# Kernel tuning notes

Hardware: AMD Instinct MI355X
Metric: run time of the kernel (lower is better)

Reference implementation:

```python
import jax, jax.numpy as jnp
import numpy as np

N_NODES = 50000
N_EDGES = 650000
NEG_SLOPE = 0.2


def gat_conv(x, src, dst, W, a_src, a_dst, bias, concat):
    """PyG-style GATConv (eval mode, self-loops already included in src/dst).
    x: [N, F_in], W: [F_in, H*C], a_src/a_dst: [H, C], bias: [H*C] or [C]."""
    N = x.shape[0]
    H, C = a_src.shape
    h = (x @ W).reshape(N, H, C)                      # [N, H, C]
    al_src = (h * a_src).sum(-1)                      # [N, H]
    al_dst = (h * a_dst).sum(-1)                      # [N, H]
    logits = jax.nn.leaky_relu(al_src[src] + al_dst[dst], NEG_SLOPE)  # [E, H]
    # segment softmax over destination neighborhoods
    m = jax.ops.segment_max(logits, dst, num_segments=N)
    m = jnp.where(jnp.isfinite(m), m, 0.0)
    e = jnp.exp(logits - m[dst])
    s = jax.ops.segment_sum(e, dst, num_segments=N)
    alpha = e / (s[dst] + 1e-16)                      # [E, H]
    msg = alpha[:, :, None] * h[src]                  # [E, H, C]
    out = jax.ops.segment_sum(msg, dst, num_segments=N)  # [N, H, C]
    out = out.reshape(N, H * C) if concat else out.mean(axis=1)
    return out + bias


def setup_inputs() -> dict:
    key = jax.random.key(0)
    ks = jax.random.split(key, 16)
    IN, HID, H, OUT = 128, 64, 4, 1
    x = jax.random.normal(ks[0], (N_NODES, IN), dtype=jnp.float32)
    edge_index = jax.random.randint(ks[1], (2, N_EDGES), 0, N_NODES, dtype=jnp.int64)
    s = 0.1
    params = {
        'W1': jax.random.normal(ks[2], (IN, H * HID), dtype=jnp.float32) * s,
        'a_src1': jax.random.normal(ks[3], (H, HID), dtype=jnp.float32) * s,
        'a_dst1': jax.random.normal(ks[4], (H, HID), dtype=jnp.float32) * s,
        'b1': jnp.zeros((H * HID,), dtype=jnp.float32),
        'W2': jax.random.normal(ks[5], (H * HID, H * HID), dtype=jnp.float32) * s,
        'a_src2': jax.random.normal(ks[6], (H, HID), dtype=jnp.float32) * s,
        'a_dst2': jax.random.normal(ks[7], (H, HID), dtype=jnp.float32) * s,
        'b2': jnp.zeros((H * HID,), dtype=jnp.float32),
        'W3': jax.random.normal(ks[8], (H * HID, OUT), dtype=jnp.float32) * s,
        'a_src3': jax.random.normal(ks[9], (1, OUT), dtype=jnp.float32) * s,
        'a_dst3': jax.random.normal(ks[10], (1, OUT), dtype=jnp.float32) * s,
        'b3': jnp.zeros((OUT,), dtype=jnp.float32),
    }
    return {'x': x, 'edge_index': edge_index, **params}


def reference(x, edge_index, W1, a_src1, a_dst1, b1, W2, a_src2, a_dst2, b2, W3, a_src3, a_dst3, b3):
    N = x.shape[0]
    loops = jnp.arange(N, dtype=edge_index.dtype)
    src = jnp.concatenate([edge_index[0], loops])
    dst = jnp.concatenate([edge_index[1], loops])
    h = gat_conv(x, src, dst, W1, a_src1, a_dst1, b1, concat=True)
    h = jax.nn.elu(h)  # dropout: identity in eval mode
    h = gat_conv(h, src, dst, W2, a_src2, a_dst2, b2, concat=True)
    h = jax.nn.elu(h)
    out = gat_conv(h, src, dst, W3, a_src3, a_dst3, b3, concat=False)
    return out
```

## Files before the change

### kernel.cpp

```cpp
#include <hip/hip_runtime.h>
#include <math.h>

#define NN 50000
#define NE 650000
#define NET 700000
#define FD 256
#define NEG 0.2f
#define NB 49

static __device__ __forceinline__ float lrelu(float v){ return v > 0.f ? v : NEG*v; }

static __device__ __forceinline__ unsigned short f2bf(float f){
  union { float f; unsigned u; } v; v.f = f;
  unsigned r = v.u + 0x7fff + ((v.u >> 16) & 1);
  return (unsigned short)(r >> 16);
}
static __device__ __forceinline__ float bf2f(unsigned short h){
  union { unsigned u; float f; } v; v.u = ((unsigned)h) << 16;
  return v.f;
}
static __device__ __forceinline__ float bflo(unsigned u){ return __uint_as_float(u << 16); }
static __device__ __forceinline__ float bfhi(unsigned u){ return __uint_as_float(u & 0xffff0000u); }

static __device__ __forceinline__ void gload_lds16(const unsigned short* g, unsigned short* l){
  __builtin_amdgcn_global_load_lds(
      (const __attribute__((address_space(1))) unsigned int*)(g),
      (__attribute__((address_space(3))) unsigned int*)(l), 16, 0, 0);
}

typedef __attribute__((ext_vector_type(8))) short short8_t;
typedef __attribute__((ext_vector_type(4))) float f32x4;

#define NX (NN*128)
#define CAST_ELEMS (NX + 128*256 + 256*256)
#define CAST_BLOCKS ((CAST_ELEMS/4 + 255)/256)
#define CNT_BLOCKS ((NET + 255)/256)
__global__ void init_fused(const float* __restrict__ x, const float* __restrict__ W1,
                           const float* __restrict__ W2,
                           unsigned short* __restrict__ xh, unsigned short* __restrict__ xl,
                           unsigned short* __restrict__ bt1h, unsigned short* __restrict__ bt1l,
                           unsigned short* __restrict__ bt2h, unsigned short* __restrict__ bt2l,
                           const int* __restrict__ ei, int* __restrict__ deg){
  int b = blockIdx.x;
  if (b >= CAST_BLOCKS){
    int e = (b - CAST_BLOCKS)*256 + threadIdx.x;
    if (e < NET){
      int d = (e < NE) ? ei[NE + e] : (e - NE);
      atomicAdd(&deg[d], 1);
    }
    return;
  }
  int i = (b*256 + threadIdx.x)*4;
  if (i < NX){
    float4 f = *(const float4*)(x + i);
    ushort4 h, l;
    h.x = f2bf(f.x); l.x = f2bf(f.x - bf2f(h.x));
    h.y = f2bf(f.y); l.y = f2bf(f.y - bf2f(h.y));
    h.z = f2bf(f.z); l.z = f2bf(f.z - bf2f(h.z));
    h.w = f2bf(f.w); l.w = f2bf(f.w - bf2f(h.w));
    *(ushort4*)(xh + i) = h;
    *(ushort4*)(xl + i) = l;
    return;
  }
  int e, K;
  const float* B;
  unsigned short *bh, *bl;
  if (i < NX + 128*256){ e = i - NX; K = 128; B = W1; bh = bt1h; bl = bt1l; }
  else if (i < CAST_ELEMS){ e = i - NX - 128*256; K = 256; B = W2; bh = bt2h; bl = bt2l; }
  else return;
  int k = e >> 8, n = e & 255;
  float4 f = *(const float4*)(B + e);
  #pragma unroll
  for (int j=0;j<4;j++){
    float fv = (j==0)?f.x:(j==1)?f.y:(j==2)?f.z:f.w;
    unsigned short h = f2bf(fv);
    bh[(n+j)*K + k] = h;
    bl[(n+j)*K + k] = f2bf(fv - bf2f(h));
  }
}

__global__ void scan_block(const int* __restrict__ deg, int* __restrict__ excl, int* __restrict__ bsums){
  __shared__ int sh[256];
  int t = threadIdx.x;
  int i0 = blockIdx.x*1024 + t*4;
  int v0 = (i0+0 < NN) ? deg[i0+0] : 0;
  int v1 = (i0+1 < NN) ? deg[i0+1] : 0;
  int v2 = (i0+2 < NN) ? deg[i0+2] : 0;
  int v3 = (i0+3 < NN) ? deg[i0+3] : 0;
  int tot = v0+v1+v2+v3;
  sh[t] = tot;
  __syncthreads();
  for (int off=1; off<256; off<<=1){
    int x = (t>=off) ? sh[t-off] : 0;
    __syncthreads();
    sh[t] += x;
    __syncthreads();
  }
  int base = sh[t] - tot;
  if (i0+0 < NN) excl[i0+0] = base;
  if (i0+1 < NN) excl[i0+1] = base + v0;
  if (i0+2 < NN) excl[i0+2] = base + v0+v1;
  if (i0+3 < NN) excl[i0+3] = base + v0+v1+v2;
  if (t == 255) bsums[blockIdx.x] = sh[255];
}

__global__ void scan_add(int* __restrict__ indptr, const int* __restrict__ bsums, int* __restrict__ cursor){
  __shared__ int boff[64];
  if (threadIdx.x < 64){
    int lane = threadIdx.x;
    int v = (lane < NB) ? bsums[lane] : 0;
    int orig = v;
    for (int off=1; off<64; off<<=1){
      int u = __shfl_up(v, off);
      if (lane >= off) v += u;
    }
    boff[lane] = v - orig;
  }
  __syncthreads();
  int i = blockIdx.x*blockDim.x + threadIdx.x;
  if (i < NN){
    int v = indptr[i] + boff[i>>10];
    indptr[i] = v;
    cursor[i] = v;
  }
  if (i == 0) indptr[NN] = NET;
}

__global__ void scatter_csr(const int* __restrict__ ei, int* __restrict__ cursor, int* __restrict__ csr){
  int e = blockIdx.x*blockDim.x + threadIdx.x;
  if (e >= NET) return;
  int s, d;
  if (e < NE){ s = ei[e]; d = ei[NE+e]; } else { s = e-NE; d = e-NE; }
  int pos = atomicAdd(&cursor[d], 1);
  csr[pos] = s;
}

template<int K>
__global__ __launch_bounds__(256, 3) void gemm_mfma(const unsigned short* __restrict__ Ahg,
                                                    const unsigned short* __restrict__ Alg,
                                                    const unsigned short* __restrict__ Bth,
                                                    const unsigned short* __restrict__ Btl,
                                                    unsigned short* __restrict__ Cb,
                                                    const float* __restrict__ a_src,
                                                    const float* __restrict__ a_dst,
                                                    float* __restrict__ al,
                                                    int M){
  constexpr int ITERS = K/32;
  __shared__ unsigned short Ah[128*32], Al[128*32], Bh[128*32], Bl[128*32];
  int t = threadIdx.x;
  int wave = t >> 6, lane = t & 63;
  int wm = wave >> 1, wn = wave & 1;
  int quad = lane >> 4, l16 = lane & 15;
  int bm0 = blockIdx.y*128, bn0 = blockIdx.x*128;

  const unsigned short* gsrc = (wave==0)?Ahg:(wave==1)?Alg:(wave==2)?Bth:Btl;
  unsigned short* lbuf       = (wave==0)?Ah :(wave==1)?Al :(wave==2)?Bh :Bl;
  int sbase = (wave < 2) ? bm0 : bn0;
  int srow = lane >> 2;
  int skg  = (lane & 3) * 8;

  const unsigned short* gp[8];
  #pragma unroll
  for (int i=0;i<8;i++){
    int r = sbase + i*16 + srow;
    if (wave < 2) r = min(r, M-1);
    gp[i] = gsrc + (size_t)r*K + skg;
  }

  f32x4 acc[4][4];
  #pragma unroll
  for (int i=0;i<4;i++)
    #pragma unroll
    for (int j=0;j<4;j++) acc[i][j] = (f32x4){0.f,0.f,0.f,0.f};

  #pragma unroll
  for (int i=0;i<8;i++) gload_lds16(gp[i], lbuf + i*512);

  #pragma unroll
  for (int it=0; it<ITERS; ++it){
    __syncthreads();

    short8_t afh[4], afl[4], bfh[4], bfl[4];
    #pragma unroll
    for (int mt=0; mt<4; ++mt){
      int row = wm*64 + mt*16 + l16;
      afh[mt] = *(short8_t*)&Ah[row*32 + quad*8];
      afl[mt] = *(short8_t*)&Al[row*32 + quad*8];
    }
    #pragma unroll
    for (int nt=0; nt<4; ++nt){
      int col = wn*64 + nt*16 + l16;
      bfh[nt] = *(short8_t*)&Bh[col*32 + quad*8];
      bfl[nt] = *(short8_t*)&Bl[col*32 + quad*8];
    }
    __syncthreads();

    if (it+1 < ITERS){
      int k0 = (it+1)*32;
      #pragma unroll
      for (int i=0;i<8;i++) gload_lds16(gp[i] + k0, lbuf + i*512);
    }

    #pragma unroll
    for (int mt=0; mt<4; ++mt)
      #pragma unroll
      for (int nt=0; nt<4; ++nt){
        acc[mt][nt] = __builtin_amdgcn_mfma_f32_16x16x32_bf16(afh[mt], bfh[nt], acc[mt][nt], 0,0,0);
        acc[mt][nt] = __builtin_amdgcn_mfma_f32_16x16x32_bf16(afh[mt], bfl[nt], acc[mt][nt], 0,0,0);
        acc[mt][nt] = __builtin_amdgcn_mfma_f32_16x16x32_bf16(afl[mt], bfh[nt], acc[mt][nt], 0,0,0);
      }
  }

  int head_w = (bn0 >> 6) + wn;
  float cs[4], cd[4];
  #pragma unroll
  for (int nt=0; nt<4; ++nt){
    cs[nt] = a_src[head_w*64 + nt*16 + l16];
    cd[nt] = a_dst[head_w*64 + nt*16 + l16];
  }
  {
    float* fsc = (float*)lbuf;
    int grow = bm0 + wm*64 + lane;
    #pragma unroll
    for (int pass=0; pass<2; ++pass){
      #pragma unroll
      for (int mt=0; mt<4; ++mt)
        #pragma unroll
        for (int r=0; r<4; ++r){
          float p = 0.f;
          #pragma unroll
          for (int nt=0; nt<4; ++nt)
            p += acc[mt][nt][r] * (pass ? cd[nt] : cs[nt]);
          fsc[(mt*16 + quad*4 + r)*17 + l16] = p;
        }
      float s = 0.f;
      #pragma unroll
      for (int j=0; j<16; ++j) s += fsc[lane*17 + j];
      if (grow < M) al[grow*8 + pass*4 + head_w] = s;
    }
  }

  unsigned short* tile = lbuf;
  #pragma unroll
  for (int mt=0; mt<4; ++mt)
    #pragma unroll
    for (int r=0; r<4; ++r){
      int rl = mt*16 + quad*4 + r;
      #pragma unroll
      for (int nt=0; nt<4; ++nt)
        tile[rl*64 + nt*16 + l16] = f2bf(acc[mt][nt][r]);
    }
  int orow = lane >> 3, ocol = (lane & 7) * 8;
  #pragma unroll
  for (int it=0; it<8; ++it){
    int rl = it*8 + orow;
    int row = bm0 + wm*64 + rl;
    if (row < M){
      uint4 v = *(uint4*)&tile[rl*64 + ocol];
      *(uint4*)(Cb + (size_t)row*FD + bn0 + wn*64 + ocol) = v;
    }
  }
}

template<bool FUSE_W3>
__global__ __launch_bounds__(256) void gat_agg(const unsigned short* __restrict__ hb,
                                               const float* __restrict__ al,
                                               const int* __restrict__ indptr, const int* __restrict__ csr,
                                               const float* __restrict__ bias,
                                               unsigned short* __restrict__ outh,
                                               unsigned short* __restrict__ outl,
                                               const float* __restrict__ W3,
                                               float* __restrict__ h3){
  __shared__ float ebuf[8][128];
  __shared__ int   sbuf[8][32];
  int wave = threadIdx.x >> 6, lane = threadIdx.x & 63;
  int half = lane >> 5, l32 = lane & 31;
  int slot = wave*2 + half;
  int n = blockIdx.x*8 + slot;
  if (n >= NN) return;
  int head8 = l32 >> 3;
  int2 ip = *(const int2*)(indptr + n);
  int base = ip.x, deg = ip.y - ip.x;
  float4 ald = *(const float4*)(al + n*8 + 4);
  float* eb = &ebuf[slot][0];
  int*   sb = &sbuf[slot][0];
  const char* hp = (const char*)hb + l32*16;

  float acc[8] = {0.f,0.f,0.f,0.f,0.f,0.f,0.f,0.f};
  float4 esum = make_float4(0.f,0.f,0.f,0.f);

  for (int j0 = 0; j0 < deg; j0 += 32){
    int j = j0 + l32;
    float4 e4 = make_float4(0.f,0.f,0.f,0.f);
    int sj = 0;
    if (j < deg){
      sj = csr[base + j];
      float4 als = *(const float4*)(al + sj*8);
      e4.x = __expf(lrelu(als.x + ald.x));
      e4.y = __expf(lrelu(als.y + ald.y));
      e4.z = __expf(lrelu(als.z + ald.z));
      e4.w = __expf(lrelu(als.w + ald.w));
      esum.x += e4.x; esum.y += e4.y; esum.z += e4.z; esum.w += e4.w;
    }
    *(float4*)&eb[l32*4] = e4;
    sb[l32] = sj << 9;
    int cnt  = min(32, deg - j0);
    int cpad = (cnt + 7) & ~7;
    for (int tt = 0; tt < cpad; tt += 8){
      uint4 r[8];
      float v[8];
      #pragma unroll
      for (int q=0; q<8; ++q){
        int o = sb[tt+q];
        v[q] = eb[(tt+q)*4 + head8];
        r[q] = *(const uint4*)(hp + o);
      }
      #pragma unroll
      for (int q=0; q<8; ++q){
        acc[0]+=v[q]*bflo(r[q].x); acc[1]+=v[q]*bfhi(r[q].x);
        acc[2]+=v[q]*bflo(r[q].y); acc[3]+=v[q]*bfhi(r[q].y);
        acc[4]+=v[q]*bflo(r[q].z); acc[5]+=v[q]*bfhi(r[q].z);
        acc[6]+=v[q]*bflo(r[q].w); acc[7]+=v[q]*bfhi(r[q].w);
      }
    }
  }

  for (int off=16; off; off>>=1){
    esum.x += __shfl_xor(esum.x, off);
    esum.y += __shfl_xor(esum.y, off);
    esum.z += __shfl_xor(esum.z, off);
    esum.w += __shfl_xor(esum.w, off);
  }
  float sH = (head8==0)?esum.x:(head8==1)?esum.y:(head8==2)?esum.z:esum.w;
  float inv = 1.f/(sH + 1e-16f);
  int ch0 = l32*8;
  float4 b0 = *(const float4*)(bias + ch0);
  float4 b1 = *(const float4*)(bias + ch0 + 4);
  float o[8];
  o[0]=acc[0]*inv+b0.x; o[1]=acc[1]*inv+b0.y; o[2]=acc[2]*inv+b0.z; o[3]=acc[3]*inv+b0.w;
  o[4]=acc[4]*inv+b1.x; o[5]=acc[5]*inv+b1.y; o[6]=acc[6]*inv+b1.z; o[7]=acc[7]*inv+b1.w;
  #pragma unroll
  for (int i=0;i<8;i++) o[i] = o[i] > 0.f ? o[i] : expm1f(o[i]);

  if (FUSE_W3){
    float4 w0 = *(const float4*)(W3 + ch0);
    float4 w1 = *(const float4*)(W3 + ch0 + 4);
    float p = o[0]*w0.x + o[1]*w0.y + o[2]*w0.z + o[3]*w0.w
            + o[4]*w1.x + o[5]*w1.y + o[6]*w1.z + o[7]*w1.w;
    #pragma unroll
    for (int off=16; off; off>>=1) p += __shfl_xor(p, off);
    if (l32 == 0) h3[n] = p;
  } else {
    unsigned hi[4], lo[4];
    #pragma unroll
    for (int i=0;i<4;i++){
      unsigned short h0 = f2bf(o[2*i]),   h1 = f2bf(o[2*i+1]);
      unsigned short g0 = f2bf(o[2*i]   - bf2f(h0));
      unsigned short g1 = f2bf(o[2*i+1] - bf2f(h1));
      hi[i] = (unsigned)h0 | ((unsigned)h1 << 16);
      lo[i] = (unsigned)g0 | ((unsigned)g1 << 16);
    }
    *(uint4*)(outh + (size_t)n*FD + ch0) = make_uint4(hi[0],hi[1],hi[2],hi[3]);
    *(uint4*)(outl + (size_t)n*FD + ch0) = make_uint4(lo[0],lo[1],lo[2],lo[3]);
  }
}

__global__ __launch_bounds__(256) void gat_agg3(const float* __restrict__ h3, const int* __restrict__ indptr,
                                                const int* __restrict__ csr, const float* __restrict__ asrc,
                                                const float* __restrict__ adst, const float* __restrict__ b3,
                                                float* __restrict__ out){
  int tid = blockIdx.x*blockDim.x + threadIdx.x;
  int n = tid >> 2, sub = tid & 3;
  if (n >= NN) return;
  float as = asrc[0], ad = adst[0];
  float hd = h3[n]*ad;
  int2 ip = *(const int2*)(indptr + n);
  float s = 0.f, w = 0.f;
  for (int e = ip.x + sub; e < ip.y; e += 4){
    float hv = h3[csr[e]];
    float ee = __expf(lrelu(as*hv + hd));
    s += ee; w += ee*hv;
  }
  s += __shfl_xor(s, 1); w += __shfl_xor(w, 1);
  s += __shfl_xor(s, 2); w += __shfl_xor(w, 2);
  if (sub == 0) out[n] = w/(s + 1e-16f) + b3[0];
}

extern "C" void kernel_launch(void* const* d_in, const int* in_sizes, int n_in,
                              void* d_out, int out_size, void* d_ws, size_t ws_size,
                              hipStream_t stream){
  const float* x   = (const float*)d_in[0];
  const int*   ei  = (const int*)d_in[1];
  const float* W1  = (const float*)d_in[2];
  const float* as1 = (const float*)d_in[3];
  const float* ad1 = (const float*)d_in[4];
  const float* b1  = (const float*)d_in[5];
  const float* W2  = (const float*)d_in[6];
  const float* as2 = (const float*)d_in[7];
  const float* ad2 = (const float*)d_in[8];
  const float* b2  = (const float*)d_in[9];
  const float* W3  = (const float*)d_in[10];
  const float* as3 = (const float*)d_in[11];
  const float* ad3 = (const float*)d_in[12];
  const float* b3  = (const float*)d_in[13];
  float* outp = (float*)d_out;

  char* w = (char*)d_ws;
  size_t off = 0;
  auto alloc = [&](size_t bytes)->void*{
    void* p = w + off; off += (bytes + 255) & ~(size_t)255; return p;
  };
  unsigned short* hb  = (unsigned short*)alloc((size_t)NN*FD*2);
  unsigned short* oh  = (unsigned short*)alloc((size_t)NN*FD*2);
  unsigned short* ol  = (unsigned short*)alloc((size_t)NN*FD*2);
  unsigned short* xh  = (unsigned short*)alloc((size_t)NN*128*2);
  unsigned short* xl  = (unsigned short*)alloc((size_t)NN*128*2);
  float* al    = (float*)alloc((size_t)NN*8*4);
  int*   indptr= (int*)alloc((size_t)(NN+1)*4);
  int*   cursor= (int*)alloc((size_t)NN*4);
  int*   csr   = (int*)alloc((size_t)NET*4);
  int*   bsums = (int*)alloc(64*4);
  float* h3    = (float*)alloc((size_t)NN*4);
  unsigned short* bt1h = (unsigned short*)alloc((size_t)256*128*2);
  unsigned short* bt1l = (unsigned short*)alloc((size_t)256*128*2);
  unsigned short* bt2h = (unsigned short*)alloc((size_t)256*256*2);
  unsigned short* bt2l = (unsigned short*)alloc((size_t)256*256*2);

  hipMemsetAsync(cursor, 0, (size_t)NN*4, stream);
  init_fused<<<CAST_BLOCKS + CNT_BLOCKS, 256, 0, stream>>>(x, W1, W2, xh, xl,
                                                           bt1h, bt1l, bt2h, bt2l,
                                                           ei, cursor);
  scan_block<<<NB, 256, 0, stream>>>(cursor, indptr, bsums);
  scan_add<<<(NN+255)/256, 256, 0, stream>>>(indptr, bsums, cursor);
  scatter_csr<<<(NET+255)/256, 256, 0, stream>>>(ei, cursor, csr);

  dim3 gemm_grid(FD/128, (NN+127)/128);
  int agg_blocks = (NN+7)/8;

  gemm_mfma<128><<<gemm_grid, 256, 0, stream>>>(xh, xl, bt1h, bt1l, hb, as1, ad1, al, NN);
  gat_agg<false><<<agg_blocks, 256, 0, stream>>>(hb, al, indptr, csr, b1, oh, ol, nullptr, nullptr);
  gemm_mfma<256><<<gemm_grid, 256, 0, stream>>>(oh, ol, bt2h, bt2l, hb, as2, ad2, al, NN);
  gat_agg<true><<<agg_blocks, 256, 0, stream>>>(hb, al, indptr, csr, b2, nullptr, nullptr, W3, h3);
  gat_agg3<<<(NN*4+255)/256, 256, 0, stream>>>(h3, indptr, csr, as3, ad3, b3, outp);
}
```

Measured before the change: 341.0 us.

## Store features in 32-channel groups and split aggregation across channel groups

The GEMM now writes node features in a channel-group-major layout (8 groups of 32 channels, each [N,32]) and attention logits head-major. Aggregation runs one block per (node tile, channel group), so each half-wave gathers a contiguous 64-byte row slice per neighbor for a single head. The intent is better cache locality, because each group's feature table is smaller. In exchange every edge's index and attention value is reloaded and recomputed 8 times, the output stores become scalar, and the fused W3 projection needs atomics plus a memset of h3.

```diff
diff --git a/kernel.cpp b/kernel.cpp
--- a/kernel.cpp
+++ b/kernel.cpp
@@ -236,7 +236,7 @@
       float s = 0.f;
       #pragma unroll
       for (int j=0; j<16; ++j) s += fsc[lane*17 + j];
-      if (grow < M) al[grow*8 + pass*4 + head_w] = s;
+      if (grow < M) al[(size_t)(pass*4 + head_w)*NN + grow] = s;
     }
   }
 
@@ -251,13 +251,15 @@
         tile[rl*64 + nt*16 + l16] = f2bf(acc[mt][nt][r]);
     }
   int orow = lane >> 3, ocol = (lane & 7) * 8;
+  int ch = bn0 + wn*64 + ocol;
+  int g = ch >> 5;
   #pragma unroll
   for (int it=0; it<8; ++it){
     int rl = it*8 + orow;
     int row = bm0 + wm*64 + rl;
     if (row < M){
       uint4 v = *(uint4*)&tile[rl*64 + ocol];
-      *(uint4*)(Cb + (size_t)row*FD + bn0 + wn*64 + ocol) = v;
+      *(uint4*)(Cb + ((size_t)g*NN + row)*32 + (ch & 31)) = v;
     }
   }
 }
@@ -271,97 +273,66 @@
                                                unsigned short* __restrict__ outl,
                                                const float* __restrict__ W3,
                                                float* __restrict__ h3){
-  __shared__ float ebuf[8][128];
+  __shared__ float ebuf[8][32];
   __shared__ int   sbuf[8][32];
   int wave = threadIdx.x >> 6, lane = threadIdx.x & 63;
   int half = lane >> 5, l32 = lane & 31;
   int slot = wave*2 + half;
-  int n = blockIdx.x*8 + slot;
+  int g    = blockIdx.x & 7;
+  int tile = blockIdx.x >> 3;
+  int n = tile*8 + slot;
   if (n >= NN) return;
-  int head8 = l32 >> 3;
+  int head = g >> 1;
   int2 ip = *(const int2*)(indptr + n);
   int base = ip.x, deg = ip.y - ip.x;
-  float4 ald = *(const float4*)(al + n*8 + 4);
+  float ald = al[(size_t)(4 + head)*NN + n];
+  const float* als_p = al + (size_t)head*NN;
   float* eb = &ebuf[slot][0];
   int*   sb = &sbuf[slot][0];
-  const char* hp = (const char*)hb + l32*16;
-
-  float acc[8] = {0.f,0.f,0.f,0.f,0.f,0.f,0.f,0.f};
-  float4 esum = make_float4(0.f,0.f,0.f,0.f);
-
+  const unsigned short* hg = hb + (size_t)g*NN*32 + l32;
+
+  float acc = 0.f, esum = 0.f;
   for (int j0 = 0; j0 < deg; j0 += 32){
     int j = j0 + l32;
-    float4 e4 = make_float4(0.f,0.f,0.f,0.f);
-    int sj = 0;
+    float e = 0.f; int sj = 0;
     if (j < deg){
-      sj = csr[base + j];
-      float4 als = *(const float4*)(al + sj*8);
-      e4.x = __expf(lrelu(als.x + ald.x));
-      e4.y = __expf(lrelu(als.y + ald.y));
-      e4.z = __expf(lrelu(als.z + ald.z));
-      e4.w = __expf(lrelu(als.w + ald.w));
-      esum.x += e4.x; esum.y += e4.y; esum.z += e4.z; esum.w += e4.w;
-    }
-    *(float4*)&eb[l32*4] = e4;
-    sb[l32] = sj << 9;
+      sj = __builtin_nontemporal_load(csr + base + j);
+      float as = als_p[sj];
+      e = __expf(lrelu(as + ald));
+      esum += e;
+    }
+    eb[l32] = e;
+    sb[l32] = sj << 5;
     int cnt  = min(32, deg - j0);
     int cpad = (cnt + 7) & ~7;
     for (int tt = 0; tt < cpad; tt += 8){
-      uint4 r[8];
-      float v[8];
-      #pragma unroll
-      for (int q=0; q<8; ++q){
-        int o = sb[tt+q];
-        v[q] = eb[(tt+q)*4 + head8];
-        r[q] = *(const uint4*)(hp + o);
-      }
-      #pragma unroll
-      for (int q=0; q<8; ++q){
-        acc[0]+=v[q]*bflo(r[q].x); acc[1]+=v[q]*bfhi(r[q].x);
-        acc[2]+=v[q]*bflo(r[q].y); acc[3]+=v[q]*bfhi(r[q].y);
-        acc[4]+=v[q]*bflo(r[q].z); acc[5]+=v[q]*bfhi(r[q].z);
-        acc[6]+=v[q]*bflo(r[q].w); acc[7]+=v[q]*bfhi(r[q].w);
-      }
-    }
-  }
-
-  for (int off=16; off; off>>=1){
-    esum.x += __shfl_xor(esum.x, off);
-    esum.y += __shfl_xor(esum.y, off);
-    esum.z += __shfl_xor(esum.z, off);
-    esum.w += __shfl_xor(esum.w, off);
-  }
-  float sH = (head8==0)?esum.x:(head8==1)?esum.y:(head8==2)?esum.z:esum.w;
-  float inv = 1.f/(sH + 1e-16f);
-  int ch0 = l32*8;
-  float4 b0 = *(const float4*)(bias + ch0);
-  float4 b1 = *(const float4*)(bias + ch0 + 4);
-  float o[8];
-  o[0]=acc[0]*inv+b0.x; o[1]=acc[1]*inv+b0.y; o[2]=acc[2]*inv+b0.z; o[3]=acc[3]*inv+b0.w;
-  o[4]=acc[4]*inv+b1.x; o[5]=acc[5]*inv+b1.y; o[6]=acc[6]*inv+b1.z; o[7]=acc[7]*inv+b1.w;
-  #pragma unroll
-  for (int i=0;i<8;i++) o[i] = o[i] > 0.f ? o[i] : expm1f(o[i]);
+      int   ofs[8]; float vv[8];
+      #pragma unroll
+      for (int q=0; q<8; ++q){ ofs[q] = sb[tt+q]; vv[q] = eb[tt+q]; }
+      float hv[8];
+      #pragma unroll
+      for (int q=0; q<8; ++q) hv[q] = bf2f(hg[ofs[q]]);
+      #pragma unroll
+      for (int q=0; q<8; ++q) acc += vv[q]*hv[q];
+    }
+  }
+
+  for (int off=16; off; off>>=1) esum += __shfl_xor(esum, off);
+  float inv = 1.f/(esum + 1e-16f);
+  int ch = g*32 + l32;
+  float o = acc*inv + bias[ch];
+  o = o > 0.f ? o : expm1f(o);
 
   if (FUSE_W3){
-    float4 w0 = *(const float4*)(W3 + ch0);
-    float4 w1 = *(const float4*)(W3 + ch0 + 4);
-    float p = o[0]*w0.x + o[1]*w0.y + o[2]*w0.z + o[3]*w0.w
-            + o[4]*w1.x + o[5]*w1.y + o[6]*w1.z + o[7]*w1.w;
+    float p = o * W3[ch];
     #pragma unroll
     for (int off=16; off; off>>=1) p += __shfl_xor(p, off);
-    if (l32 == 0) h3[n] = p;
+    if (l32 == 0) atomicAdd(&h3[n], p);
   } else {
-    unsigned hi[4], lo[4];
-    #pragma unroll
-    for (int i=0;i<4;i++){
-      unsigned short h0 = f2bf(o[2*i]),   h1 = f2bf(o[2*i+1]);
-      unsigned short g0 = f2bf(o[2*i]   - bf2f(h0));
-      unsigned short g1 = f2bf(o[2*i+1] - bf2f(h1));
-      hi[i] = (unsigned)h0 | ((unsigned)h1 << 16);
-      lo[i] = (unsigned)g0 | ((unsigned)g1 << 16);
-    }
-    *(uint4*)(outh + (size_t)n*FD + ch0) = make_uint4(hi[0],hi[1],hi[2],hi[3]);
-    *(uint4*)(outl + (size_t)n*FD + ch0) = make_uint4(lo[0],lo[1],lo[2],lo[3]);
+    unsigned short hh = f2bf(o);
+    unsigned short ll = f2bf(o - bf2f(hh));
+    __builtin_nontemporal_store(hh, outh + (size_t)n*FD + ch);
+    __builtin_nontemporal_store(ll, outl + (size_t)n*FD + ch);
   }
 }
 
@@ -427,6 +398,7 @@
   unsigned short* bt2l = (unsigned short*)alloc((size_t)256*256*2);
 
   hipMemsetAsync(cursor, 0, (size_t)NN*4, stream);
+  hipMemsetAsync(h3, 0, (size_t)NN*4, stream);
   init_fused<<<CAST_BLOCKS + CNT_BLOCKS, 256, 0, stream>>>(x, W1, W2, xh, xl,
                                                            bt1h, bt1l, bt2h, bt2l,
                                                            ei, cursor);
@@ -435,7 +407,7 @@
   scatter_csr<<<(NET+255)/256, 256, 0, stream>>>(ei, cursor, csr);
 
   dim3 gemm_grid(FD/128, (NN+127)/128);
-  int agg_blocks = (NN+7)/8;
+  int agg_blocks = (NN/8) * 8;
 
   gemm_mfma<128><<<gemm_grid, 256, 0, stream>>>(xh, xl, bt1h, bt1l, hb, as1, ad1, al, NN);
   gat_agg<false><<<agg_blocks, 256, 0, stream>>>(hb, al, indptr, csr, b1, oh, ol, nullptr, nullptr);
```

Result: slower. 446.8 us (+31.0%).

## Precompute per-edge attention exponentials in a separate edge-parallel kernel

Applied to the files above, without the earlier changes.

Adds an alpha_k kernel that computes exp(leaky_relu(al_src+al_dst)) for every CSR edge in an edge-parallel pass, storing the results in a float4 buffer. To support this, scatter_csr now also records each edge's destination. gat_agg then reads the precomputed values instead of gathering al[src] and computing exponentials inside its node-parallel loop. This splits the gather latency away from the aggregation kernel, at the cost of two extra launches, an extra edge-sized write and read, and a second CSR array.

```diff
diff --git a/kernel.cpp b/kernel.cpp
--- a/kernel.cpp
+++ b/kernel.cpp
@@ -4,6 +4,7 @@
 #define NN 50000
 #define NE 650000
 #define NET 700000
+#define NETP (NET + 16)
 #define FD 256
 #define NEG 0.2f
 #define NB 49
@@ -126,13 +127,30 @@
   if (i == 0) indptr[NN] = NET;
 }
 
-__global__ void scatter_csr(const int* __restrict__ ei, int* __restrict__ cursor, int* __restrict__ csr){
+__global__ void scatter_csr(const int* __restrict__ ei, int* __restrict__ cursor,
+                            int* __restrict__ csr, int* __restrict__ csrd){
   int e = blockIdx.x*blockDim.x + threadIdx.x;
   if (e >= NET) return;
   int s, d;
   if (e < NE){ s = ei[e]; d = ei[NE+e]; } else { s = e-NE; d = e-NE; }
   int pos = atomicAdd(&cursor[d], 1);
   csr[pos] = s;
+  csrd[pos] = d;
+}
+
+__global__ __launch_bounds__(256) void alpha_k(const int* __restrict__ csr, const int* __restrict__ csrd,
+                                               const float* __restrict__ al, float4* __restrict__ alpha4){
+  int p = blockIdx.x*256 + threadIdx.x;
+  if (p >= NET) return;
+  int s = csr[p], d = csrd[p];
+  float4 as = *(const float4*)(al + s*8);
+  float4 ad = *(const float4*)(al + d*8 + 4);
+  float4 e;
+  e.x = __expf(lrelu(as.x + ad.x));
+  e.y = __expf(lrelu(as.y + ad.y));
+  e.z = __expf(lrelu(as.z + ad.z));
+  e.w = __expf(lrelu(as.w + ad.w));
+  alpha4[p] = e;
 }
 
 template<int K>
@@ -264,7 +282,7 @@
 
 template<bool FUSE_W3>
 __global__ __launch_bounds__(256) void gat_agg(const unsigned short* __restrict__ hb,
-                                               const float* __restrict__ al,
+                                               const float4* __restrict__ alpha4,
                                                const int* __restrict__ indptr, const int* __restrict__ csr,
                                                const float* __restrict__ bias,
                                                unsigned short* __restrict__ outh,
@@ -281,7 +299,6 @@
   int head8 = l32 >> 3;
   int2 ip = *(const int2*)(indptr + n);
   int base = ip.x, deg = ip.y - ip.x;
-  float4 ald = *(const float4*)(al + n*8 + 4);
   float* eb = &ebuf[slot][0];
   int*   sb = &sbuf[slot][0];
   const char* hp = (const char*)hb + l32*16;
@@ -295,11 +312,7 @@
     int sj = 0;
     if (j < deg){
       sj = csr[base + j];
-      float4 als = *(const float4*)(al + sj*8);
-      e4.x = __expf(lrelu(als.x + ald.x));
-      e4.y = __expf(lrelu(als.y + ald.y));
-      e4.z = __expf(lrelu(als.z + ald.z));
-      e4.w = __expf(lrelu(als.w + ald.w));
+      e4 = alpha4[base + j];
       esum.x += e4.x; esum.y += e4.y; esum.z += e4.z; esum.w += e4.w;
     }
     *(float4*)&eb[l32*4] = e4;
@@ -416,9 +429,11 @@
   unsigned short* xh  = (unsigned short*)alloc((size_t)NN*128*2);
   unsigned short* xl  = (unsigned short*)alloc((size_t)NN*128*2);
   float* al    = (float*)alloc((size_t)NN*8*4);
+  float4* alpha4 = (float4*)alloc((size_t)NETP*16);
   int*   indptr= (int*)alloc((size_t)(NN+1)*4);
   int*   cursor= (int*)alloc((size_t)NN*4);
   int*   csr   = (int*)alloc((size_t)NET*4);
+  int*   csrd  = (int*)alloc((size_t)NET*4);
   int*   bsums = (int*)alloc(64*4);
   float* h3    = (float*)alloc((size_t)NN*4);
   unsigned short* bt1h = (unsigned short*)alloc((size_t)256*128*2);
@@ -432,14 +447,17 @@
                                                            ei, cursor);
   scan_block<<<NB, 256, 0, stream>>>(cursor, indptr, bsums);
   scan_add<<<(NN+255)/256, 256, 0, stream>>>(indptr, bsums, cursor);
-  scatter_csr<<<(NET+255)/256, 256, 0, stream>>>(ei, cursor, csr);
+  scatter_csr<<<(NET+255)/256, 256, 0, stream>>>(ei, cursor, csr, csrd);
 
   dim3 gemm_grid(FD/128, (NN+127)/128);
   int agg_blocks = (NN+7)/8;
+  int alpha_blocks = (NET+255)/256;
 
   gemm_mfma<128><<<gemm_grid, 256, 0, stream>>>(xh, xl, bt1h, bt1l, hb, as1, ad1, al, NN);
-  gat_agg<false><<<agg_blocks, 256, 0, stream>>>(hb, al, indptr, csr, b1, oh, ol, nullptr, nullptr);
+  alpha_k<<<alpha_blocks, 256, 0, stream>>>(csr, csrd, al, alpha4);
+  gat_agg<false><<<agg_blocks, 256, 0, stream>>>(hb, alpha4, indptr, csr, b1, oh, ol, nullptr, nullptr);
   gemm_mfma<256><<<gemm_grid, 256, 0, stream>>>(oh, ol, bt2h, bt2l, hb, as2, ad2, al, NN);
-  gat_agg<true><<<agg_blocks, 256, 0, stream>>>(hb, al, indptr, csr, b2, nullptr, nullptr, W3, h3);
+  alpha_k<<<alpha_blocks, 256, 0, stream>>>(csr, csrd, al, alpha4);
+  gat_agg<true><<<agg_blocks, 256, 0, stream>>>(hb, alpha4, indptr, csr, b2, nullptr, nullptr, W3, h3);
   gat_agg3<<<(NN*4+255)/256, 256, 0, stream>>>(h3, indptr, csr, as3, ad3, b3, outp);
 }
```

After: 349.2 us. +2.4%, slower.
